# Performance work log

Measured on AMD Instinct MI355X. Metric: run time of the kernel, lower is better.

Reference implementation:

```python
import jax, jax.numpy as jnp
import numpy as np

B, L, BERT_DIM = 8, 1024, 1024
HEADS, HEAD_SIZE = 12, 64


def setup_inputs() -> dict:
    key = jax.random.key(0)
    k1, k2, k3, k4, k5, k6 = jax.random.split(key, 6)
    s = 1.0 / np.sqrt(BERT_DIM)
    return {
        "head": jax.random.normal(k1, (B, L, BERT_DIM), dtype=jnp.float32),
        "tail": jax.random.normal(k2, (B, L, BERT_DIM), dtype=jnp.float32),
        "W_head": jax.random.normal(k3, (BERT_DIM, HEADS * HEAD_SIZE), dtype=jnp.float32) * s,
        "b_head": jax.random.normal(k4, (HEADS * HEAD_SIZE,), dtype=jnp.float32) * 0.01,
        "W_tail": jax.random.normal(k5, (BERT_DIM, HEADS * HEAD_SIZE), dtype=jnp.float32) * s,
        "b_tail": jax.random.normal(k6, (HEADS * HEAD_SIZE,), dtype=jnp.float32) * 0.01,
    }


def _sincos(seq_len, dim, dtype):
    # SinusoidalPositionEmbedding with merge_mode='zero': (L, dim), interleaved [sin, cos]
    pos = jnp.arange(seq_len, dtype=dtype)                     # (L,)
    inv = jnp.power(10000.0, -2.0 * jnp.arange(dim // 2, dtype=dtype) / dim)  # (dim/2,)
    ang = pos[:, None] * inv[None, :]                          # (L, dim/2)
    emb = jnp.stack([jnp.sin(ang), jnp.cos(ang)], axis=-1).reshape(seq_len, dim)
    # cos_pos: even/odd duplication as in torch reference
    cos_pos = jnp.repeat(emb[:, 1::2], 2, axis=-1)             # (L, dim)
    sin_pos = jnp.repeat(emb[:, 0::2], 2, axis=-1)             # (L, dim)
    return cos_pos, sin_pos


def _rotate_half(x):
    # stack([-x[...,1::2], x[...,::2]], -1).reshape(x.shape)
    return jnp.stack([-x[..., 1::2], x[..., 0::2]], axis=-1).reshape(x.shape)


def reference(head, tail, W_head, b_head, W_tail, b_tail):
    bsz, seq_len, _ = head.shape
    h = (head @ W_head + b_head).reshape(bsz, seq_len, HEADS, HEAD_SIZE)
    t = (tail @ W_tail + b_tail).reshape(bsz, seq_len, HEADS, HEAD_SIZE)

    cos_pos, sin_pos = _sincos(seq_len, HEAD_SIZE, h.dtype)
    cos_pos = cos_pos[None, :, None, :]  # (1, L, 1, D)
    sin_pos = sin_pos[None, :, None, :]

    h = h * cos_pos + _rotate_half(h) * sin_pos
    t = t * cos_pos + _rotate_half(t) * sin_pos

    # (B, H, L, L)
    logits = jnp.einsum("blhd,bmhd->bhlm", h, t)
    return logits / jnp.sqrt(jnp.asarray(HEAD_SIZE, h.dtype))
```

## Files before the change

### kernel.cpp

```cpp
#include <hip/hip_runtime.h>
#include <hip/hip_bf16.h>


#define DIM   1024
#define NOUT  768
#define NHEAD 12

typedef __attribute__((ext_vector_type(8))) short bf16x8;
typedef __attribute__((ext_vector_type(4))) float f32x4;

__device__ __forceinline__ ushort f2bf(float f) {
  union { float f; unsigned u; } v; v.f = f;
  unsigned r = v.u + 0x7fffu + ((v.u >> 16) & 1u);
  return (ushort)(r >> 16);
}

__device__ __forceinline__ void gload16(const ushort* g, ushort* l) {
  __builtin_amdgcn_global_load_lds(
      (const __attribute__((address_space(1))) unsigned int*)g,
      (__attribute__((address_space(3))) unsigned int*)l, 16, 0, 0);
}

__global__ __launch_bounds__(256) void prep_kernel(
    const float* __restrict__ head, const float* __restrict__ tail,
    const float* __restrict__ Wh,   const float* __restrict__ Wt_,
    ushort* __restrict__ Hx, ushort* __restrict__ Tx,
    ushort* __restrict__ WtH, ushort* __restrict__ WtT,
    float2* __restrict__ rope)
{
  __shared__ ushort lds[64][72];
  const int bx = blockIdx.x, tid = threadIdx.x;

  if (bx < 4096) {
    size_t t = (size_t)bx * 256 + tid;
    const float* src; ushort* dst; size_t e;
    if (t < 524288) { src = head; dst = Hx; e = t * 16; }
    else            { src = tail; dst = Tx; e = (t - 524288) * 16; }
    const float4* p = reinterpret_cast<const float4*>(src + e);
    float4 a = p[0], b = p[1], c = p[2], d = p[3];
    ushort o[16] = { f2bf(a.x), f2bf(a.y), f2bf(a.z), f2bf(a.w),
                     f2bf(b.x), f2bf(b.y), f2bf(b.z), f2bf(b.w),
                     f2bf(c.x), f2bf(c.y), f2bf(c.z), f2bf(c.w),
                     f2bf(d.x), f2bf(d.y), f2bf(d.z), f2bf(d.w) };
    *reinterpret_cast<bf16x8*>(dst + e)     = *reinterpret_cast<bf16x8*>(o);
    *reinterpret_cast<bf16x8*>(dst + e + 8) = *reinterpret_cast<bf16x8*>(o + 8);
  } else if (bx < 4480) {
    int t2 = bx - 4096;
    int wsel = t2 / 192, tile = t2 % 192;
    int k0 = (tile / 12) * 64, n0 = (tile % 12) * 64;
    const float* W = wsel ? Wt_ : Wh;
    ushort* WT = wsel ? WtT : WtH;
#pragma unroll
    for (int q = 0; q < 16; ++q) {
      int idx = q * 256 + tid;
      int kr = idx >> 6, nc = idx & 63;
      lds[nc][kr] = f2bf(W[(size_t)(k0 + kr) * NOUT + n0 + nc]);
    }
    __syncthreads();
#pragma unroll
    for (int q = 0; q < 2; ++q) {
      int idx = q * 256 + tid;
      int nc = idx >> 3, kg = idx & 7;
      *reinterpret_cast<bf16x8*>(&WT[(size_t)(n0 + nc) * DIM + k0 + kg * 8]) =
          *reinterpret_cast<bf16x8*>(&lds[nc][kg * 8]);
    }
  } else {
    int j = (bx - 4480) * 256 + tid;
    int l = j >> 5, i = j & 31;
    float inv = powf(10000.0f, -(float)i / 32.0f);
    float ang = (float)l * inv;
    rope[j] = make_float2(cosf(ang), sinf(ang));
  }
}

__global__ __launch_bounds__(256) void proj_rope_kernel(
    const ushort* __restrict__ Hx,  const ushort* __restrict__ Tx,
    const ushort* __restrict__ WtH, const ushort* __restrict__ WtT,
    const float*  __restrict__ bh,  const float*  __restrict__ bt,
    const float2* __restrict__ rope,
    ushort* __restrict__ Hb, ushort* __restrict__ Tb)
{
  const bool sel = (blockIdx.z != 0);
  const ushort* X    = sel ? Tx  : Hx;
  const ushort* Wt   = sel ? WtT : WtH;
  const float*  bias = sel ? bt  : bh;
  ushort*       Out  = sel ? Tb  : Hb;

  __shared__ ushort As[128 * 64];
  __shared__ ushort Bs[128 * 64];

  const int tid = threadIdx.x;
  const int m0 = blockIdx.x * 128;
  const int n0 = blockIdx.y * 128;
  const int wid = tid >> 6, lane = tid & 63;
  const int wm = wid >> 1, wn = wid & 1;
  const int r = lane & 15, g = lane >> 4;
  const int r7 = r & 7;

  f32x4 acc[4][4] = {};

  for (int k0 = 0; k0 < DIM; k0 += 64) {
#pragma unroll
    for (int i = 0; i < 4; ++i) {
      int task = i * 256 + tid;
      int row = task >> 3, c = task & 7;
      int csrc = c ^ (row & 7);
      gload16(X + (size_t)(m0 + row) * DIM + k0 + csrc * 8, &As[task * 8]);
    }
#pragma unroll
    for (int i = 0; i < 4; ++i) {
      int task = i * 256 + tid;
      int row = task >> 3, c = task & 7;
      int csrc = c ^ (row & 7);
      gload16(Wt + (size_t)(n0 + row) * DIM + k0 + csrc * 8, &Bs[task * 8]);
    }
    __syncthreads();

    bf16x8 af[2][4], bfv[2][4];
#pragma unroll
    for (int ks = 0; ks < 2; ++ks) {
      int cs = (ks * 4 + g) ^ r7;
#pragma unroll
      for (int m = 0; m < 4; ++m)
        af[ks][m] = *reinterpret_cast<const bf16x8*>(
            &As[(wm * 64 + m * 16 + r) * 64 + cs * 8]);
#pragma unroll
      for (int n = 0; n < 4; ++n)
        bfv[ks][n] = *reinterpret_cast<const bf16x8*>(
            &Bs[(wn * 64 + n * 16 + r) * 64 + cs * 8]);
    }
#pragma unroll
    for (int n = 0; n < 4; ++n)
#pragma unroll
      for (int m = 0; m < 4; ++m) {
        acc[n][m] = __builtin_amdgcn_mfma_f32_16x16x32_bf16(
            bfv[0][n], af[0][m], acc[n][m], 0, 0, 0);
        acc[n][m] = __builtin_amdgcn_mfma_f32_16x16x32_bf16(
            bfv[1][n], af[1][m], acc[n][m], 0, 0, 0);
      }
    __syncthreads();
  }

#pragma unroll
  for (int n = 0; n < 4; ++n) {
    int col = n0 + wn * 64 + n * 16 + g * 4;
    int hd = col >> 6, dd = col & 63;
    int ii = dd >> 1;
    float4 bs4 = *reinterpret_cast<const float4*>(&bias[col]);
#pragma unroll
    for (int m = 0; m < 4; ++m) {
      int grow = m0 + wm * 64 + m * 16 + r;
      int l = grow & 1023, b = grow >> 10;
      float4 rp = *reinterpret_cast<const float4*>(&rope[l * 32 + ii]);
      float v0 = acc[n][m][0] + bs4.x;
      float v1 = acc[n][m][1] + bs4.y;
      float v2 = acc[n][m][2] + bs4.z;
      float v3 = acc[n][m][3] + bs4.w;
      ushort o[4] = { f2bf(v0 * rp.x - v1 * rp.y),
                      f2bf(v1 * rp.x + v0 * rp.y),
                      f2bf(v2 * rp.z - v3 * rp.w),
                      f2bf(v3 * rp.z + v2 * rp.w) };
      *reinterpret_cast<ushort4*>(
          &Out[(((size_t)b * NHEAD + hd) * 1024 + l) * 64 + dd]) =
          *reinterpret_cast<ushort4*>(o);
    }
  }
}

__global__ __launch_bounds__(256) void logits_kernel(
    const ushort* __restrict__ Hb, const ushort* __restrict__ Tb,
    float* __restrict__ out)
{
  const int f = blockIdx.x;
  const int rx = f & 7, q = f >> 3;
  const int j = q & 63, zq = q >> 6;
  const int z = zq * 8 + rx;
  const int l0 = (j >> 3) * 128, m0 = (j & 7) * 128;

  const int tid = threadIdx.x;
  const int wid = tid >> 6, lane = tid & 63;
  const int wl = wid >> 1, wm = wid & 1;
  const int r = lane & 15, g = lane >> 4;
  const size_t zo = (size_t)z << 16;
  const ushort* H = Hb + zo;
  const ushort* T = Tb + zo;
  float* C = out + ((size_t)z << 20);

  bf16x8 tf[4][2], hf[4][2];
#pragma unroll
  for (int t = 0; t < 4; ++t)
#pragma unroll
    for (int ks = 0; ks < 2; ++ks) {
      tf[t][ks] = *reinterpret_cast<const bf16x8*>(
          T + (m0 + wm * 64 + t * 16 + r) * 64 + ks * 32 + g * 8);
      hf[t][ks] = *reinterpret_cast<const bf16x8*>(
          H + (l0 + wl * 64 + t * 16 + r) * 64 + ks * 32 + g * 8);
    }

  f32x4 acc[4][4] = {};
#pragma unroll
  for (int mt = 0; mt < 4; ++mt)
#pragma unroll
    for (int lt = 0; lt < 4; ++lt) {
      acc[mt][lt] = __builtin_amdgcn_mfma_f32_16x16x32_bf16(
          tf[mt][0], hf[lt][0], acc[mt][lt], 0, 0, 0);
      acc[mt][lt] = __builtin_amdgcn_mfma_f32_16x16x32_bf16(
          tf[mt][1], hf[lt][1], acc[mt][lt], 0, 0, 0);
    }

#pragma unroll
  for (int lt = 0; lt < 4; ++lt)
#pragma unroll
    for (int mt = 0; mt < 4; ++mt) {
      int l = l0 + wl * 64 + lt * 16 + r;
      int m = m0 + wm * 64 + mt * 16 + g * 4;
      f32x4 v = acc[mt][lt] * 0.125f;
      *reinterpret_cast<f32x4*>(&C[(size_t)l * 1024 + m]) = v;
    }
}

extern "C" void kernel_launch(void* const* d_in, const int* in_sizes, int n_in,
                              void* d_out, int out_size, void* d_ws, size_t ws_size,
                              hipStream_t stream)
{
  const float* head   = (const float*)d_in[0];
  const float* tail   = (const float*)d_in[1];
  const float* W_head = (const float*)d_in[2];
  const float* b_head = (const float*)d_in[3];
  const float* W_tail = (const float*)d_in[4];
  const float* b_tail = (const float*)d_in[5];
  float* out = (float*)d_out;

  char* ws = (char*)d_ws;
  ushort* WtH  = (ushort*)(ws);
  ushort* WtT  = (ushort*)(ws + 1572864);
  float2* rope = (float2*)(ws + 3145728);
  ushort* Hb   = (ushort*)(ws + 3407872);
  ushort* Tb   = (ushort*)(ws + 15990784);

  ushort* Hx = (ushort*)d_out;
  ushort* Tx = Hx + 8388608;

  prep_kernel<<<dim3(4608), dim3(256), 0, stream>>>(
      head, tail, W_head, W_tail, Hx, Tx, WtH, WtT, rope);
  proj_rope_kernel<<<dim3(64, 6, 2), dim3(256), 0, stream>>>(
      Hx, Tx, WtH, WtT, b_head, b_tail, rope, Hb, Tb);
  logits_kernel<<<dim3(6144), dim3(256), 0, stream>>>(Hb, Tb, out);
}
```

Baseline: 161.2 us.

## Retile logits kernel to full-row 32xL strips with streamed T fragments

Each logits block now covers 32 query rows by all 1024 key columns instead of a 128x128 tile. Each wave keeps its H fragments in registers and streams 16 T fragments from global memory, writing each output tile right after its MFMAs. This lowers register pressure, which may raise occupancy, and writes whole contiguous output rows per block, which should help the store-bound fp32 output. The cost is that the T data is re-read more often across blocks and the grid has fewer blocks.

```diff
diff --git a/kernel.cpp b/kernel.cpp
--- a/kernel.cpp
+++ b/kernel.cpp
@@ -173,50 +173,41 @@
 {
   const int f = blockIdx.x;
   const int rx = f & 7, q = f >> 3;
-  const int j = q & 63, zq = q >> 6;
+  const int zq = q >> 5, lg = q & 31;
   const int z = zq * 8 + rx;
-  const int l0 = (j >> 3) * 128, m0 = (j & 7) * 128;
+  const int l0 = lg * 32;
 
   const int tid = threadIdx.x;
-  const int wid = tid >> 6, lane = tid & 63;
-  const int wl = wid >> 1, wm = wid & 1;
+  const int w = tid >> 6, lane = tid & 63;
   const int r = lane & 15, g = lane >> 4;
   const size_t zo = (size_t)z << 16;
-  const ushort* H = Hb + zo;
-  const ushort* T = Tb + zo;
-  float* C = out + ((size_t)z << 20);
-
-  bf16x8 tf[4][2], hf[4][2];
-#pragma unroll
-  for (int t = 0; t < 4; ++t)
-#pragma unroll
-    for (int ks = 0; ks < 2; ++ks) {
-      tf[t][ks] = *reinterpret_cast<const bf16x8*>(
-          T + (m0 + wm * 64 + t * 16 + r) * 64 + ks * 32 + g * 8);
-      hf[t][ks] = *reinterpret_cast<const bf16x8*>(
-          H + (l0 + wl * 64 + t * 16 + r) * 64 + ks * 32 + g * 8);
-    }
-
-  f32x4 acc[4][4] = {};
-#pragma unroll
-  for (int mt = 0; mt < 4; ++mt)
-#pragma unroll
-    for (int lt = 0; lt < 4; ++lt) {
-      acc[mt][lt] = __builtin_amdgcn_mfma_f32_16x16x32_bf16(
-          tf[mt][0], hf[lt][0], acc[mt][lt], 0, 0, 0);
-      acc[mt][lt] = __builtin_amdgcn_mfma_f32_16x16x32_bf16(
-          tf[mt][1], hf[lt][1], acc[mt][lt], 0, 0, 0);
-    }
-
-#pragma unroll
-  for (int lt = 0; lt < 4; ++lt)
-#pragma unroll
-    for (int mt = 0; mt < 4; ++mt) {
-      int l = l0 + wl * 64 + lt * 16 + r;
-      int m = m0 + wm * 64 + mt * 16 + g * 4;
-      f32x4 v = acc[mt][lt] * 0.125f;
-      *reinterpret_cast<f32x4*>(&C[(size_t)l * 1024 + m]) = v;
-    }
+  const ushort* Hp = Hb + zo + (size_t)(l0 + r) * 64 + g * 8;
+  const ushort* Tp = Tb + zo + (size_t)(w * 256 + r) * 64 + g * 8;
+  float* C = out + ((size_t)z << 20) + w * 256;
+
+  bf16x8 hf[2][2];
+#pragma unroll
+  for (int lt = 0; lt < 2; ++lt)
+#pragma unroll
+    for (int ks = 0; ks < 2; ++ks)
+      hf[lt][ks] = *reinterpret_cast<const bf16x8*>(
+          Hp + lt * 16 * 64 + ks * 32);
+
+#pragma unroll
+  for (int mt = 0; mt < 16; ++mt) {
+    bf16x8 t0 = *reinterpret_cast<const bf16x8*>(Tp + mt * 1024);
+    bf16x8 t1 = *reinterpret_cast<const bf16x8*>(Tp + mt * 1024 + 32);
+    f32x4 a0 = {}, a1 = {};
+    a0 = __builtin_amdgcn_mfma_f32_16x16x32_bf16(t0, hf[0][0], a0, 0, 0, 0);
+    a0 = __builtin_amdgcn_mfma_f32_16x16x32_bf16(t1, hf[0][1], a0, 0, 0, 0);
+    a1 = __builtin_amdgcn_mfma_f32_16x16x32_bf16(t0, hf[1][0], a1, 0, 0, 0);
+    a1 = __builtin_amdgcn_mfma_f32_16x16x32_bf16(t1, hf[1][1], a1, 0, 0, 0);
+    int mloc = mt * 16 + g * 4;
+    *reinterpret_cast<f32x4*>(
+        &C[(size_t)(l0 + 0 * 16 + r) * 1024 + mloc]) = a0 * 0.125f;
+    *reinterpret_cast<f32x4*>(
+        &C[(size_t)(l0 + 1 * 16 + r) * 1024 + mloc]) = a1 * 0.125f;
+  }
 }
 
 extern "C" void kernel_launch(void* const* d_in, const int* in_sizes, int n_in,
@@ -245,5 +236,5 @@
       head, tail, W_head, W_tail, Hx, Tx, WtH, WtT, rope);
   proj_rope_kernel<<<dim3(64, 6, 2), dim3(256), 0, stream>>>(
       Hx, Tx, WtH, WtT, b_head, b_tail, rope, Hb, Tb);
-  logits_kernel<<<dim3(6144), dim3(256), 0, stream>>>(Hb, Tb, out);
-}
+  logits_kernel<<<dim3(3072), dim3(256), 0, stream>>>(Hb, Tb, out);
+}
```

Result: slower. 166.4 us (+3.2%).
